# Performance work log

Hardware: AMD Instinct MI355X
Metric: run time of the kernel (lower is better)

The kernel has to match this reference:

```python
import jax, jax.numpy as jnp
import numpy as np


def setup_inputs() -> dict:
    key = jax.random.key(0)
    k1, k2, k3, k4 = jax.random.split(key, 4)
    b, c, h, w = 4, 256, 64, 64
    Fq_l = jax.random.normal(k1, (b, c, h, w), dtype=jnp.float32)
    Fp_l = jax.random.normal(k2, (b, c, h, w), dtype=jnp.float32)
    # 1x1 conv: weight [out=c//2, in=c], bias [c//2]
    W = jax.random.normal(k3, (c // 2, c), dtype=jnp.float32) * (1.0 / np.sqrt(c))
    bias = jax.random.normal(k4, (c // 2,), dtype=jnp.float32) * 0.01
    return {"Fq_l": Fq_l, "Fp_l": Fp_l, "W": W, "bias": bias}


def reference(Fq_l, Fp_l, W, bias):
    b, c, h, w = Fq_l.shape
    hw = h * w
    # 1x1 conv == per-pixel linear projection
    q = jnp.einsum('oc,bchw->bohw', W, Fq_l) + bias[None, :, None, None]
    p = jnp.einsum('oc,bchw->bohw', W, Fp_l) + bias[None, :, None, None]
    qf = q.reshape(b, -1, hw)  # [b, c/2, hw]
    pf = p.reshape(b, -1, hw)
    qf = qf / jnp.linalg.norm(qf, axis=1, keepdims=True)
    pf = pf / jnp.linalg.norm(pf, axis=1, keepdims=True)
    # cosine similarity, [b, hw, hw]
    sim = jnp.einsum('bcn,bcm->bnm', qf, pf)
    idx = jnp.argmax(sim, axis=-1)  # [b, hw]
    Fp_flat = Fp_l.reshape(b, c, hw)
    aligned = jnp.take_along_axis(Fp_flat, idx[:, None, :], axis=2)  # [b, c, hw]
    return aligned.reshape(b, c, h, w)
```

## Files before the change

### kernel.cpp

```cpp
#include <hip/hip_runtime.h>

#define HW 4096
#define LCAP 1536

typedef short bf16x8 __attribute__((ext_vector_type(8)));
typedef float f32x16 __attribute__((ext_vector_type(16)));

__device__ __forceinline__ ushort f2bf_rne(float f) {
    unsigned u = __float_as_uint(f);
    return (ushort)((u + 0x7FFFu + ((u >> 16) & 1u)) >> 16);
}

__global__ __launch_bounds__(256) void transpose_w_kernel(
    const float* __restrict__ Wm, float* __restrict__ Wt)
{
    const int o = blockIdx.x;
    const int c = threadIdx.x;
    Wt[c * 128 + o] = Wm[o * 256 + c];
}

__global__ __launch_bounds__(256) void proj_kernel(
    const float* __restrict__ Fq, const float* __restrict__ Fp,
    const float* __restrict__ Wt, const float* __restrict__ bias,
    float* __restrict__ Qt, float* __restrict__ Pt,
    ushort* __restrict__ Qpk, ushort* __restrict__ Ppk,
    float* __restrict__ qnorm)
{
    __shared__ float Ws[64][128];
    __shared__ float Xs[64][64];
    __shared__ float psum[16][68];

    const int tid = threadIdx.x;
    const int z  = blockIdx.z;
    const float* __restrict__ X = z ? Fp : Fq;
    const int b  = blockIdx.y;
    const int n0 = blockIdx.x * 64;
    const int og = tid >> 4;
    const int ng = tid & 15;

    float acc[4][8];
    #pragma unroll
    for (int i = 0; i < 4; ++i)
        #pragma unroll
        for (int j = 0; j < 8; ++j) acc[i][j] = 0.f;

    for (int cc = 0; cc < 4; ++cc) {
        __syncthreads();
        {
            const float4* src = (const float4*)(Wt + (size_t)cc * 64 * 128);
            float4* dst = (float4*)Ws;
            #pragma unroll
            for (int it = 0; it < 8; ++it) dst[it * 256 + tid] = src[it * 256 + tid];
        }
        #pragma unroll
        for (int it = 0; it < 4; ++it) {
            int f = it * 256 + tid;
            int r = f >> 4, n4 = f & 15;
            *(float4*)&Xs[r][n4 * 4] =
                *(const float4*)&X[(size_t)(b * 256 + cc * 64 + r) * HW + n0 + n4 * 4];
        }
        __syncthreads();

        for (int r = 0; r < 64; ++r) {
            float4 w0 = *(const float4*)&Ws[r][og * 8];
            float4 w1 = *(const float4*)&Ws[r][og * 8 + 4];
            float4 xv = *(const float4*)&Xs[r][ng * 4];
            float wa[8] = {w0.x, w0.y, w0.z, w0.w, w1.x, w1.y, w1.z, w1.w};
            float xa[4] = {xv.x, xv.y, xv.z, xv.w};
            #pragma unroll
            for (int i = 0; i < 4; ++i)
                #pragma unroll
                for (int j = 0; j < 8; ++j)
                    acc[i][j] += wa[j] * xa[i];
        }
    }

    {
        float4 b0 = *(const float4*)&bias[og * 8];
        float4 b1 = *(const float4*)&bias[og * 8 + 4];
        float ba[8] = {b0.x, b0.y, b0.z, b0.w, b1.x, b1.y, b1.z, b1.w};
        #pragma unroll
        for (int i = 0; i < 4; ++i)
            #pragma unroll
            for (int j = 0; j < 8; ++j) acc[i][j] += ba[j];
    }

    #pragma unroll
    for (int i = 0; i < 4; ++i) {
        float s = 0.f;
        #pragma unroll
        for (int j = 0; j < 8; ++j) s += acc[i][j] * acc[i][j];
        psum[og][ng * 4 + i] = s;
    }
    __syncthreads();
    float tot[4];
    #pragma unroll
    for (int i = 0; i < 4; ++i) {
        float s = 0.f;
        #pragma unroll
        for (int g = 0; g < 16; ++g) s += psum[g][ng * 4 + i];
        tot[i] = s;
    }

    if (z) {
        #pragma unroll
        for (int i = 0; i < 4; ++i) {
            float s = 1.0f / sqrtf(tot[i]);
            #pragma unroll
            for (int j = 0; j < 8; ++j) acc[i][j] *= s;
        }
    } else if (og == 0) {
        #pragma unroll
        for (int i = 0; i < 4; ++i)
            qnorm[b * HW + n0 + ng * 4 + i] = sqrtf(tot[i]);
    }

    {
        float* __restrict__ T = z ? Pt : Qt;
        #pragma unroll
        for (int i = 0; i < 4; ++i) {
            size_t tb = ((size_t)b * HW + n0 + ng * 4 + i) * 128 + og * 8;
            *(float4*)&T[tb]     = make_float4(acc[i][0], acc[i][1], acc[i][2], acc[i][3]);
            *(float4*)&T[tb + 4] = make_float4(acc[i][4], acc[i][5], acc[i][6], acc[i][7]);
        }
    }
    {
        ushort* __restrict__ PK = z ? Ppk : Qpk;
        const int ks = og >> 1;
        #pragma unroll
        for (int i = 0; i < 4; ++i) {
            const int na  = n0 + ng * 4 + i;
            const int t32 = na >> 5;
            const int lt  = (na & 31) + 32 * (og & 1);
            ushort u[8];
            #pragma unroll
            for (int k = 0; k < 8; ++k) u[k] = f2bf_rne(acc[i][k]);
            size_t pk = ((((size_t)b * 128 + t32) * 8 + ks) * 64 + lt) * 8;
            uint4 w;
            w.x = (unsigned)u[0] | ((unsigned)u[1] << 16);
            w.y = (unsigned)u[2] | ((unsigned)u[3] << 16);
            w.z = (unsigned)u[4] | ((unsigned)u[5] << 16);
            w.w = (unsigned)u[6] | ((unsigned)u[7] << 16);
            *(uint4*)&PK[pk] = w;
        }
    }
}

__global__ __launch_bounds__(256, 4) void sim_sketch_kernel(
    const ushort* __restrict__ Qpk, const ushort* __restrict__ Ppk,
    const float* __restrict__ qnorm,
    float* __restrict__ Vmax, unsigned char* __restrict__ SK,
    unsigned char* __restrict__ CM)
{
    __shared__ ushort Bs[16384];

    const int tid  = threadIdx.x;
    const int lane = tid & 63;
    const int w    = tid >> 6;
    const int nb   = blockIdx.x;
    const int b    = blockIdx.y;
    const int ms   = blockIdx.z;
    const int hi   = lane >> 5;

    {
        const uint4* src = (const uint4*)(Ppk + ((size_t)(b * 128 + ms * 4)) * 4096);
        uint4* dst = (uint4*)Bs;
        #pragma unroll
        for (int it = 0; it < 8; ++it) dst[it * 256 + tid] = src[it * 256 + tid];
    }

    const ushort* __restrict__ qbase =
        Qpk + ((size_t)(b * 128 + nb * 4)) * 4096 + (size_t)lane * 8;
    bf16x8 qf[8];
    #pragma unroll
    for (int ks = 0; ks < 8; ++ks)
        qf[ks] = *(const bf16x8*)(qbase + (w * 8 + ks) * 512);

    float rq[16];
    #pragma unroll
    for (int r = 0; r < 16; ++r) {
        int nl_ = (r & 3) + 8 * (r >> 2) + 4 * hi;
        rq[r] = 256.0f / qnorm[b * HW + nb * 128 + w * 32 + nl_];
    }

    const size_t g16f = (size_t)b * 256 + (size_t)(nb * 4 + w) * 2 + hi;
    const int mb0 = ms * 128 + (lane & 31);

    float bestv[16];
    #pragma unroll
    for (int r = 0; r < 16; ++r) bestv[r] = -1e30f;

    __syncthreads();

    #pragma unroll 2
    for (int mtl = 0; mtl < 4; ++mtl) {
        f32x16 acc;
        #pragma unroll
        for (int r = 0; r < 16; ++r) acc[r] = 0.f;
        #pragma unroll
        for (int ks = 0; ks < 8; ++ks) {
            bf16x8 bb = *(const bf16x8*)&Bs[((mtl * 8 + ks) * 64 + lane) * 8];
            acc = __builtin_amdgcn_mfma_f32_32x32x16_bf16(qf[ks], bb, acc, 0, 0, 0);
        }
        #pragma unroll
        for (int r = 0; r < 16; ++r)
            bestv[r] = fmaxf(bestv[r], acc[r]);

        float x[16];
        #pragma unroll
        for (int r = 0; r < 16; ++r) x[r] = acc[r] * rq[r];

        float c0 = fmaxf(fmaxf(fmaxf(x[0], x[1]), fmaxf(x[2], x[3])),
                         fmaxf(fmaxf(x[4], x[5]), fmaxf(x[6], x[7])));
        float c1 = fmaxf(fmaxf(fmaxf(x[8], x[9]), fmaxf(x[10], x[11])),
                         fmaxf(fmaxf(x[12], x[13]), fmaxf(x[14], x[15])));
        int cmi = (int)(fmaxf(c0, c1) + 0.5f) + 1;
        cmi = cmi < 0 ? 0 : (cmi > 255 ? 255 : cmi);

        unsigned dw[4] = {0u, 0u, 0u, 0u};
        #pragma unroll
        for (int r = 0; r < 16; ++r) {
#if __has_builtin(__builtin_amdgcn_cvt_pk_u8_f32)
            dw[r >> 2] = (unsigned)__builtin_amdgcn_cvt_pk_u8_f32(
                x[r], (unsigned)(r & 3), (int)dw[r >> 2]);
#else
            int vi = (int)rintf(x[r]);
            vi = vi < 0 ? 0 : (vi > 255 ? 255 : vi);
            dw[r >> 2] |= (unsigned)vi << (8 * (r & 3));
#endif
        }
        const int m = mb0 + mtl * 32;
        uint4 pk;
        pk.x = dw[0]; pk.y = dw[1]; pk.z = dw[2]; pk.w = dw[3];
        *(uint4*)(SK + ((g16f * 4096 + (size_t)m) << 4)) = pk;
        CM[g16f * 4096 + (size_t)m] = (unsigned char)cmi;
    }

    #pragma unroll
    for (int r = 0; r < 16; ++r) {
        float v = bestv[r];
        #pragma unroll
        for (int d = 1; d < 32; d <<= 1)
            v = fmaxf(v, __shfl_xor(v, d, 64));
        if ((lane & 31) == 0) {
            int nl_ = (r & 3) + 8 * (r >> 2) + 4 * hi;
            int na = nb * 128 + w * 32 + nl_;
            Vmax[((size_t)b * HW + na) * 32 + ms] = v;
        }
    }
}

__device__ __noinline__ void dot_one_slow(
    const float* Qsrow, const float* __restrict__ Pt,
    int b, int m, int n, unsigned long long* __restrict__ best)
{
    const float4* __restrict__ pr = (const float4*)&Pt[((size_t)b * HW + m) * 128];
    float acc = 0.f;
    #pragma unroll
    for (int k = 0; k < 32; ++k) {
        float4 pv = pr[k];
        float4 qv = *(const float4*)&Qsrow[k * 4];
        acc += qv.x * pv.x + qv.y * pv.y + qv.z * pv.z + qv.w * pv.w;
    }
    unsigned u = __float_as_uint(acc);
    unsigned kk = (u & 0x80000000u) ? ~u : (u | 0x80000000u);
    unsigned long long key = ((unsigned long long)kk << 32) | (unsigned)(4095 - m);
    atomicMax(&best[(size_t)b * HW + n], key);
}

__global__ __launch_bounds__(256) void scan_rescore_kernel(
    const unsigned char* __restrict__ SK, const unsigned char* __restrict__ CM,
    const float* __restrict__ Vmax, const float* __restrict__ qnorm,
    const float* __restrict__ Qt, const float* __restrict__ Pt,
    unsigned long long* __restrict__ best)
{
    __shared__ float Qs[16][132];
    __shared__ int nlist[16];
    __shared__ int t8s[16];
    __shared__ ushort hl[LCAP];
    __shared__ unsigned lcnt;

    const int fg  = blockIdx.x;
    const int tid = threadIdx.x;
    const int b = fg >> 8, g = fg & 255, t = g >> 1, gs = g & 1;

    if (tid == 0) lcnt = 0u;
    if (tid < 16) {
        int n = t * 32 + (tid & 3) + 8 * (tid >> 2) + 4 * gs;
        nlist[tid] = n;
        best[(size_t)b * HW + n] = 0ull;
        float gmax = -1e30f;
        const float4* vs = (const float4*)&Vmax[((size_t)b * HW + n) * 32];
        #pragma unroll
        for (int s = 0; s < 8; ++s) {
            float4 v = vs[s];
            gmax = fmaxf(gmax, fmaxf(fmaxf(v.x, v.y), fmaxf(v.z, v.w)));
        }
        float qn  = qnorm[b * HW + n];
        float thr = gmax - (0.016f * qn + 1e-6f);
        int tt = (int)floorf(thr * (256.0f / qn)) - 1;
        t8s[tid] = tt < 0 ? 0 : (tt > 255 ? 255 : tt);
    }
    __syncthreads();

    #pragma unroll
    for (int it = 0; it < 2; ++it) {
        int idx = it * 256 + tid;
        int row = idx >> 5, c4 = (idx & 31) * 4;
        *(float4*)&Qs[row][c4] =
            *(const float4*)&Qt[((size_t)b * HW + nlist[row]) * 128 + c4];
    }

    int myt[16];
    #pragma unroll
    for (int j = 0; j < 16; ++j) myt[j] = t8s[j];
    int gmin = myt[0];
    #pragma unroll
    for (int j = 1; j < 16; ++j) gmin = min(gmin, myt[j]);
    __syncthreads();

    const unsigned char* __restrict__ cmrow = CM + ((size_t)fg << 12);
    const unsigned char* __restrict__ skrow = SK + ((size_t)fg << 16);

    #pragma unroll
    for (int it = 0; it < 4; ++it) {
        int m0 = (it * 256 + tid) * 4;
        unsigned cm4 = *(const unsigned*)(cmrow + m0);
        #pragma unroll
        for (int k = 0; k < 4; ++k) {
            int cmv = (int)((cm4 >> (8 * k)) & 255u);
            if (cmv >= gmin) {
                int m = m0 + k;
                uint4 v = *(const uint4*)(skrow + ((size_t)m << 4));
                unsigned wv[4] = {v.x, v.y, v.z, v.w};
                #pragma unroll
                for (int d = 0; d < 4; ++d) {
                    #pragma unroll
                    for (int kk = 0; kk < 4; ++kk) {
                        int bv = (int)((wv[d] >> (8 * kk)) & 255u);
                        int j = d * 4 + kk;
                        if (bv >= myt[j]) {
                            unsigned pos = atomicAdd(&lcnt, 1u);
                            if (pos < LCAP) {
                                hl[pos] = (ushort)((j << 12) | m);
                            } else {
                                dot_one_slow(&Qs[j][0], Pt, b, m, nlist[j], best);
                            }
                        }
                    }
                }
            }
        }
    }

    __syncthreads();
    unsigned cnt = lcnt < LCAP ? lcnt : LCAP;
    for (unsigned p = tid; p < cnt; p += 256) {
        int e = hl[p];
        int j = e >> 12, m = e & 4095;
        const float4* __restrict__ pr = (const float4*)&Pt[((size_t)b * HW + m) * 128];
        float acc = 0.f;
        #pragma unroll
        for (int k = 0; k < 32; ++k) {
            float4 pv = pr[k];
            float4 qv = *(const float4*)&Qs[j][k * 4];
            acc += qv.x * pv.x + qv.y * pv.y + qv.z * pv.z + qv.w * pv.w;
        }
        unsigned u = __float_as_uint(acc);
        unsigned kk = (u & 0x80000000u) ? ~u : (u | 0x80000000u);
        unsigned long long key = ((unsigned long long)kk << 32) | (unsigned)(4095 - m);
        atomicMax(&best[(size_t)b * HW + nlist[j]], key);
    }
}

__global__ __launch_bounds__(256) void gather_kernel(
    const float* __restrict__ Fp, const unsigned long long* __restrict__ best,
    float* __restrict__ out)
{
    __shared__ float row[4096];
    const int blk = blockIdx.x;
    const int c = blk & 255;
    const int b = blk >> 8;
    const int tid = threadIdx.x;

    const float* __restrict__ src = Fp + ((size_t)b * 256 + c) * HW;
    #pragma unroll
    for (int it = 0; it < 4; ++it) {
        int f = it * 256 + tid;
        *(float4*)&row[f * 4] = *(const float4*)&src[f * 4];
    }
    __syncthreads();

    float* __restrict__ dst = out + ((size_t)b * 256 + c) * HW;
    #pragma unroll
    for (int it = 0; it < 16; ++it) {
        int n = it * 256 + tid;
        int m = 4095 - (int)(best[(size_t)b * HW + n] & 0xFFFull);
        dst[n] = row[m];
    }
}

extern "C" void kernel_launch(void* const* d_in, const int* in_sizes, int n_in,
                              void* d_out, int out_size, void* d_ws, size_t ws_size,
                              hipStream_t stream) {
    const float* Fq   = (const float*)d_in[0];
    const float* Fp   = (const float*)d_in[1];
    const float* Wm   = (const float*)d_in[2];
    const float* bias = (const float*)d_in[3];
    float* out = (float*)d_out;

    char* base = (char*)d_ws;
    float*  Qt    = (float*)(base);
    float*  Pt    = (float*)(base + (8u << 20));
    ushort* Qpk   = (ushort*)(base + (16u << 20));
    ushort* Ppk   = (ushort*)(base + (20u << 20));
    unsigned char* SK = (unsigned char*)(base + (24u << 20));
    unsigned char* CM = (unsigned char*)(base + (88u << 20));
    char* x = base + (92u << 20);
    float*  qnorm = (float*)x;              x += 65536;
    float*  Vmax  = (float*)x;              x += 2097152;
    unsigned long long* best = (unsigned long long*)x; x += 131072;
    float*  Wtg   = (float*)x;

    transpose_w_kernel<<<128, 256, 0, stream>>>(Wm, Wtg);
    proj_kernel<<<dim3(64, 4, 2), 256, 0, stream>>>(Fq, Fp, Wtg, bias,
                                                    Qt, Pt, Qpk, Ppk, qnorm);
    sim_sketch_kernel<<<dim3(32, 4, 32), 256, 0, stream>>>(Qpk, Ppk, qnorm,
                                                           Vmax, SK, CM);
    scan_rescore_kernel<<<1024, 256, 0, stream>>>(SK, CM, Vmax, qnorm,
                                                  Qt, Pt, best);
    gather_kernel<<<1024, 256, 0, stream>>>(Fp, best, out);
}
```

Baseline: 179.6 us.

## Widen projection tile, split MFMA accumulator chains, pack chunk-max bytes

The projection kernel now computes 128 pixels per block with an 8x8 register tile per thread, halving the grid and doubling reuse of the staged weights. The sim-sketch kernel splits its eight dependent MFMAs into two independent accumulator chains to shorten the dependency stall, then sums them. It also packs the four per-tile chunk-max bytes into one 32-bit store instead of four byte stores. The scan kernel's index mapping is changed to match the new chunk-max layout. Costs are more registers in the projection kernel, only 256 projection blocks, and an extra add pass over the accumulators.

After: 243.7 us. +35.7%, slower.

```diff
diff --git a/kernel.cpp b/kernel.cpp
--- a/kernel.cpp
+++ b/kernel.cpp
@@ -27,20 +27,20 @@
     float* __restrict__ qnorm)
 {
     __shared__ float Ws[64][128];
-    __shared__ float Xs[64][64];
-    __shared__ float psum[16][68];
+    __shared__ float Xs[64][128];
+    __shared__ float psum[16][137];
 
     const int tid = threadIdx.x;
     const int z  = blockIdx.z;
     const float* __restrict__ X = z ? Fp : Fq;
     const int b  = blockIdx.y;
-    const int n0 = blockIdx.x * 64;
+    const int n0 = blockIdx.x * 128;
     const int og = tid >> 4;
     const int ng = tid & 15;
 
-    float acc[4][8];
-    #pragma unroll
-    for (int i = 0; i < 4; ++i)
+    float acc[8][8];
+    #pragma unroll
+    for (int i = 0; i < 8; ++i)
         #pragma unroll
         for (int j = 0; j < 8; ++j) acc[i][j] = 0.f;
 
@@ -53,9 +53,9 @@
             for (int it = 0; it < 8; ++it) dst[it * 256 + tid] = src[it * 256 + tid];
         }
         #pragma unroll
-        for (int it = 0; it < 4; ++it) {
+        for (int it = 0; it < 8; ++it) {
             int f = it * 256 + tid;
-            int r = f >> 4, n4 = f & 15;
+            int r = f >> 5, n4 = f & 31;
             *(float4*)&Xs[r][n4 * 4] =
                 *(const float4*)&X[(size_t)(b * 256 + cc * 64 + r) * HW + n0 + n4 * 4];
         }
@@ -64,11 +64,12 @@
         for (int r = 0; r < 64; ++r) {
             float4 w0 = *(const float4*)&Ws[r][og * 8];
             float4 w1 = *(const float4*)&Ws[r][og * 8 + 4];
-            float4 xv = *(const float4*)&Xs[r][ng * 4];
+            float4 x0 = *(const float4*)&Xs[r][ng * 8];
+            float4 x1 = *(const float4*)&Xs[r][ng * 8 + 4];
             float wa[8] = {w0.x, w0.y, w0.z, w0.w, w1.x, w1.y, w1.z, w1.w};
-            float xa[4] = {xv.x, xv.y, xv.z, xv.w};
+            float xa[8] = {x0.x, x0.y, x0.z, x0.w, x1.x, x1.y, x1.z, x1.w};
             #pragma unroll
-            for (int i = 0; i < 4; ++i)
+            for (int i = 0; i < 8; ++i)
                 #pragma unroll
                 for (int j = 0; j < 8; ++j)
                     acc[i][j] += wa[j] * xa[i];
@@ -80,46 +81,46 @@
         float4 b1 = *(const float4*)&bias[og * 8 + 4];
         float ba[8] = {b0.x, b0.y, b0.z, b0.w, b1.x, b1.y, b1.z, b1.w};
         #pragma unroll
-        for (int i = 0; i < 4; ++i)
+        for (int i = 0; i < 8; ++i)
             #pragma unroll
             for (int j = 0; j < 8; ++j) acc[i][j] += ba[j];
     }
 
     #pragma unroll
-    for (int i = 0; i < 4; ++i) {
+    for (int i = 0; i < 8; ++i) {
         float s = 0.f;
         #pragma unroll
         for (int j = 0; j < 8; ++j) s += acc[i][j] * acc[i][j];
-        psum[og][ng * 4 + i] = s;
-    }
-    __syncthreads();
-    float tot[4];
-    #pragma unroll
-    for (int i = 0; i < 4; ++i) {
+        psum[og][ng * 8 + i] = s;
+    }
+    __syncthreads();
+    float tot[8];
+    #pragma unroll
+    for (int i = 0; i < 8; ++i) {
         float s = 0.f;
         #pragma unroll
-        for (int g = 0; g < 16; ++g) s += psum[g][ng * 4 + i];
+        for (int g = 0; g < 16; ++g) s += psum[g][ng * 8 + i];
         tot[i] = s;
     }
 
     if (z) {
         #pragma unroll
-        for (int i = 0; i < 4; ++i) {
+        for (int i = 0; i < 8; ++i) {
             float s = 1.0f / sqrtf(tot[i]);
             #pragma unroll
             for (int j = 0; j < 8; ++j) acc[i][j] *= s;
         }
     } else if (og == 0) {
         #pragma unroll
-        for (int i = 0; i < 4; ++i)
-            qnorm[b * HW + n0 + ng * 4 + i] = sqrtf(tot[i]);
+        for (int i = 0; i < 8; ++i)
+            qnorm[b * HW + n0 + ng * 8 + i] = sqrtf(tot[i]);
     }
 
     {
         float* __restrict__ T = z ? Pt : Qt;
         #pragma unroll
-        for (int i = 0; i < 4; ++i) {
-            size_t tb = ((size_t)b * HW + n0 + ng * 4 + i) * 128 + og * 8;
+        for (int i = 0; i < 8; ++i) {
+            size_t tb = ((size_t)b * HW + n0 + ng * 8 + i) * 128 + og * 8;
             *(float4*)&T[tb]     = make_float4(acc[i][0], acc[i][1], acc[i][2], acc[i][3]);
             *(float4*)&T[tb + 4] = make_float4(acc[i][4], acc[i][5], acc[i][6], acc[i][7]);
         }
@@ -128,8 +129,8 @@
         ushort* __restrict__ PK = z ? Ppk : Qpk;
         const int ks = og >> 1;
         #pragma unroll
-        for (int i = 0; i < 4; ++i) {
-            const int na  = n0 + ng * 4 + i;
+        for (int i = 0; i < 8; ++i) {
+            const int na  = n0 + ng * 8 + i;
             const int t32 = na >> 5;
             const int lt  = (na & 31) + 32 * (og & 1);
             ushort u[8];
@@ -190,25 +191,33 @@
     #pragma unroll
     for (int r = 0; r < 16; ++r) bestv[r] = -1e30f;
 
+    unsigned cmw = 0u;
+
     __syncthreads();
 
     #pragma unroll 2
     for (int mtl = 0; mtl < 4; ++mtl) {
-        f32x16 acc;
-        #pragma unroll
-        for (int r = 0; r < 16; ++r) acc[r] = 0.f;
-        #pragma unroll
-        for (int ks = 0; ks < 8; ++ks) {
+        f32x16 a0, a1;
+        #pragma unroll
+        for (int r = 0; r < 16; ++r) { a0[r] = 0.f; a1[r] = 0.f; }
+        #pragma unroll
+        for (int ks = 0; ks < 4; ++ks) {
             bf16x8 bb = *(const bf16x8*)&Bs[((mtl * 8 + ks) * 64 + lane) * 8];
-            acc = __builtin_amdgcn_mfma_f32_32x32x16_bf16(qf[ks], bb, acc, 0, 0, 0);
-        }
-        #pragma unroll
-        for (int r = 0; r < 16; ++r)
-            bestv[r] = fmaxf(bestv[r], acc[r]);
+            a0 = __builtin_amdgcn_mfma_f32_32x32x16_bf16(qf[ks], bb, a0, 0, 0, 0);
+        }
+        #pragma unroll
+        for (int ks = 4; ks < 8; ++ks) {
+            bf16x8 bb = *(const bf16x8*)&Bs[((mtl * 8 + ks) * 64 + lane) * 8];
+            a1 = __builtin_amdgcn_mfma_f32_32x32x16_bf16(qf[ks], bb, a1, 0, 0, 0);
+        }
 
         float x[16];
         #pragma unroll
-        for (int r = 0; r < 16; ++r) x[r] = acc[r] * rq[r];
+        for (int r = 0; r < 16; ++r) {
+            float s = a0[r] + a1[r];
+            bestv[r] = fmaxf(bestv[r], s);
+            x[r] = s * rq[r];
+        }
 
         float c0 = fmaxf(fmaxf(fmaxf(x[0], x[1]), fmaxf(x[2], x[3])),
                          fmaxf(fmaxf(x[4], x[5]), fmaxf(x[6], x[7])));
@@ -216,6 +225,7 @@
                          fmaxf(fmaxf(x[12], x[13]), fmaxf(x[14], x[15])));
         int cmi = (int)(fmaxf(c0, c1) + 0.5f) + 1;
         cmi = cmi < 0 ? 0 : (cmi > 255 ? 255 : cmi);
+        cmw |= (unsigned)cmi << (8 * mtl);
 
         unsigned dw[4] = {0u, 0u, 0u, 0u};
         #pragma unroll
@@ -233,8 +243,9 @@
         uint4 pk;
         pk.x = dw[0]; pk.y = dw[1]; pk.z = dw[2]; pk.w = dw[3];
         *(uint4*)(SK + ((g16f * 4096 + (size_t)m) << 4)) = pk;
-        CM[g16f * 4096 + (size_t)m] = (unsigned char)cmi;
-    }
+    }
+
+    *(unsigned*)(CM + g16f * 4096 + ms * 128 + (lane & 31) * 4) = cmw;
 
     #pragma unroll
     for (int r = 0; r < 16; ++r) {
@@ -324,13 +335,14 @@
 
     #pragma unroll
     for (int it = 0; it < 4; ++it) {
-        int m0 = (it * 256 + tid) * 4;
-        unsigned cm4 = *(const unsigned*)(cmrow + m0);
+        int p0 = (it * 256 + tid) * 4;
+        int mbase = (p0 & ~127) + ((p0 >> 2) & 31);
+        unsigned cm4 = *(const unsigned*)(cmrow + p0);
         #pragma unroll
         for (int k = 0; k < 4; ++k) {
             int cmv = (int)((cm4 >> (8 * k)) & 255u);
             if (cmv >= gmin) {
-                int m = m0 + k;
+                int m = mbase + k * 32;
                 uint4 v = *(const uint4*)(skrow + ((size_t)m << 4));
                 unsigned wv[4] = {v.x, v.y, v.z, v.w};
                 #pragma unroll
@@ -423,7 +435,7 @@
     float*  Wtg   = (float*)x;
 
     transpose_w_kernel<<<128, 256, 0, stream>>>(Wm, Wtg);
-    proj_kernel<<<dim3(64, 4, 2), 256, 0, stream>>>(Fq, Fp, Wtg, bias,
+    proj_kernel<<<dim3(32, 4, 2), 256, 0, stream>>>(Fq, Fp, Wtg, bias,
                                                     Qt, Pt, Qpk, Ppk, qnorm);
     sim_sketch_kernel<<<dim3(32, 4, 32), 256, 0, stream>>>(Qpk, Ppk, qnorm,
                                                            Vmax, SK, CM);
```
